# Optimization experiments

Measured on AMD Instinct MI355X. Metric: run time of the kernel, lower is better.

## Reference

```python
import jax, jax.numpy as jnp
import numpy as np

DIM = 192
HEADS = 4
CTX = 256
HID = int(DIM * 2.66)  # 510


def _dwconv(x, w):
    # x: (b,c,h,w), w: (c,1,3,3) depthwise
    return jax.lax.conv_general_dilated(
        x, w, window_strides=(1, 1), padding='SAME',
        dimension_numbers=('NCHW', 'OIHW', 'NCHW'),
        feature_group_count=x.shape[1])


def _conv1x1(x, w):
    # w: (out, in)
    return jnp.einsum('oc,bchw->bohw', w, x)


def _layernorm(x, weight, bias):
    # WithBias LayerNorm over channel dim (last dim after to_3d == channels)
    mu = x.mean(axis=1, keepdims=True)
    var = ((x - mu) ** 2).mean(axis=1, keepdims=True)
    xn = (x - mu) / jnp.sqrt(var + 1e-5)
    return xn * weight[None, :, None, None] + bias[None, :, None, None]


def setup_inputs() -> dict:
    key = jax.random.key(0)
    ks = jax.random.split(key, 16)
    s = 0.02
    inp = {
        'x': jax.random.normal(ks[0], (8, DIM, 128, 128), jnp.float32),
        'context_emb': jax.random.normal(ks[1], (8, CTX), jnp.float32),
        'ln1_w': jnp.ones((DIM,), jnp.float32),
        'ln1_b': jnp.zeros((DIM,), jnp.float32),
        'ln2_w': jnp.ones((DIM,), jnp.float32),
        'ln2_b': jnp.zeros((DIM,), jnp.float32),
        'w_qkv': jax.random.normal(ks[2], (3 * DIM, DIM), jnp.float32) * s,
        'w_qkv_dw': jax.random.normal(ks[3], (3 * DIM, 1, 3, 3), jnp.float32) * s,
        'w_proj': jax.random.normal(ks[4], (DIM, DIM), jnp.float32) * s,
        'base_temp': jnp.ones((HEADS, 1, 1), jnp.float32),
        'ta_w1': jax.random.normal(ks[5], (DIM // 4, CTX), jnp.float32) * s,
        'ta_b1': jnp.zeros((DIM // 4,), jnp.float32),
        'ta_w2': jax.random.normal(ks[6], (HEADS, DIM // 4), jnp.float32) * s,
        'ta_b2': jnp.zeros((HEADS,), jnp.float32),
        'vg_w': jax.random.normal(ks[7], (DIM, CTX), jnp.float32) * s,
        'vg_b': jnp.zeros((DIM,), jnp.float32),
        'w_local': jax.random.normal(ks[8], (DIM, 1, 3, 3), jnp.float32) * s,
        'w_ffn_in': jax.random.normal(ks[9], (2 * HID, DIM), jnp.float32) * s,
        'w_ffn_dw': jax.random.normal(ks[10], (2 * HID, 1, 3, 3), jnp.float32) * s,
        'w_ffn_out': jax.random.normal(ks[11], (DIM, HID), jnp.float32) * s,
    }
    return inp


def _forward(x, context_emb, ln1_w, ln1_b, ln2_w, ln2_b, w_qkv, w_qkv_dw,
             w_proj, base_temp, ta_w1, ta_b1, ta_w2, ta_b2, vg_w, vg_b,
             w_local, w_ffn_in, w_ffn_dw, w_ffn_out):
    b, c, h, w = x.shape
    hd = c // HEADS
    scale = hd ** (-0.5)

    # ---- Attention branch ----
    residual = x
    xn = _layernorm(x, ln1_w, ln1_b)

    # context adapters
    t = jax.nn.relu(context_emb @ ta_w1.T + ta_b1) @ ta_w2.T + ta_b2  # (b,heads)
    temp_factor = jax.nn.sigmoid(t)[:, :, None, None] * 2.0 + 0.5    # (b,heads,1,1)
    total_temp = base_temp[None] * temp_factor
    v_gate = jax.nn.sigmoid(context_emb @ vg_w.T + vg_b)             # (b,dim)
    v_gate = v_gate.reshape(b, HEADS, hd, 1)

    qkv = _dwconv(_conv1x1(xn, w_qkv), w_qkv_dw)
    q, k, v = jnp.split(qkv, 3, axis=1)

    def heads_flat(t4):
        return t4.reshape(b, HEADS, hd, h * w)

    qf = heads_flat(q)
    kf = heads_flat(k)
    vf = heads_flat(v)
    qf = qf / jnp.maximum(jnp.linalg.norm(qf, axis=-1, keepdims=True), 1e-12)
    kf = kf / jnp.maximum(jnp.linalg.norm(kf, axis=-1, keepdims=True), 1e-12)

    attn = jnp.einsum('bhcn,bhdn->bhcd', qf, kf) * scale  # (b,heads,hd,hd)
    attn = jax.nn.softmax(attn * total_temp, axis=-1)

    out_global = jnp.einsum('bhcd,bhdn->bhcn', attn, vf * v_gate)
    out_global = out_global.reshape(b, c, h, w)
    out_local = _dwconv(v, w_local)
    x = residual + _conv1x1(out_global + out_local, w_proj)

    # ---- GDFN branch ----
    residual = x
    xn = _layernorm(x, ln2_w, ln2_b)
    y = _dwconv(_conv1x1(xn, w_ffn_in), w_ffn_dw)
    y1, y2 = jnp.split(y, 2, axis=1)
    y = jax.nn.gelu(y1, approximate=False) * y2
    x = residual + _conv1x1(y, w_ffn_out)
    return x


def reference(x, context_emb, ln1_w, ln1_b, ln2_w, ln2_b, w_qkv, w_qkv_dw,
              w_proj, base_temp, ta_w1, ta_b1, ta_w2, ta_b2, vg_w, vg_b,
              w_local, w_ffn_in, w_ffn_dw, w_ffn_out):
    return _forward(x, context_emb, ln1_w, ln1_b, ln2_w, ln2_b, w_qkv,
                    w_qkv_dw, w_proj, base_temp, ta_w1, ta_b1, ta_w2, ta_b2,
                    vg_w, vg_b, w_local, w_ffn_in, w_ffn_dw, w_ffn_out)
```

## Files before the change

kernel.cpp:

```cpp
#include <hip/hip_runtime.h>
#include <math.h>

#define NB 8
#define NC 192
#define NH 128
#define NW 128
#define HW 16384
#define NQ 576
#define NHID 510
#define NHIDP 512
#define NG2 1020
#define NG2P 1024

#define BROWS 32
#define BSLOTS 34
#define BPIX (BSLOTS * NW)
#define BIPIX (BROWS * NW)

typedef unsigned short u16;
typedef short s16x8 __attribute__((ext_vector_type(8)));
typedef float f32x4 __attribute__((ext_vector_type(4)));

#define MFMA_BF16(a, b, c) __builtin_amdgcn_mfma_f32_16x16x32_bf16((a), (b), (c), 0, 0, 0)

__device__ __forceinline__ u16 f2bf(float f) {
  union { float f; unsigned u; } v; v.f = f;
  unsigned r = v.u + 0x7fffu + ((v.u >> 16) & 1u);
  return (u16)(r >> 16);
}
__device__ __forceinline__ float bf2f(u16 h) {
  union { unsigned u; float f; } v; v.u = ((unsigned)h) << 16; return v.f;
}
__device__ __forceinline__ float lo2f(unsigned u) {
  union { unsigned u; float f; } v; v.u = u << 16; return v.f;
}
__device__ __forceinline__ float hi2f(unsigned u) {
  union { unsigned u; float f; } v; v.u = u & 0xffff0000u; return v.f;
}

__device__ __forceinline__ void gll16(const void* g, void* l) {
  __builtin_amdgcn_global_load_lds(
      (const __attribute__((address_space(1))) void*)g,
      (__attribute__((address_space(3))) void*)l, 16, 0, 0);
}

__global__ void k_prep(const float* __restrict__ wq, const float* __restrict__ wfi,
                       const float* __restrict__ wfo,
                       u16* __restrict__ oq, u16* __restrict__ ofi, u16* __restrict__ ofo) {
  const int n1 = NQ * NC, n2 = NG2P * NC, n3 = NC * NHIDP;
  for (int i = blockIdx.x * blockDim.x + threadIdx.x; i < n1 + n2 + n3;
       i += gridDim.x * blockDim.x) {
    if (i < n1) {
      oq[i] = f2bf(wq[i]);
    } else if (i < n1 + n2) {
      int j = i - n1; int row = j / NC;
      u16 v = 0;
      if (row < NG2) v = f2bf(wfi[j]);
      ofi[j] = v;
    } else {
      int j = i - n1 - n2; int row = j >> 9, col = j & 511;
      u16 v = 0;
      if (col < NHID) v = f2bf(wfo[row * NHID + col]);
      ofo[j] = v;
    }
  }
}

__global__ void k_ctx(const float* __restrict__ ce, const float* __restrict__ taw1,
                      const float* __restrict__ tab1, const float* __restrict__ taw2,
                      const float* __restrict__ tab2, const float* __restrict__ vgw,
                      const float* __restrict__ vgb, const float* __restrict__ btemp,
                      float* __restrict__ tempt, float* __restrict__ vg) {
  int b = blockIdx.x, t = threadIdx.x;
  __shared__ float sce[256];
  __shared__ float shid[48];
  sce[t] = ce[b * 256 + t];
  __syncthreads();
  if (t < 48) {
    float s = tab1[t];
    for (int j = 0; j < 256; j++) s = fmaf(taw1[t * 256 + j], sce[j], s);
    shid[t] = fmaxf(s, 0.f);
  }
  __syncthreads();
  if (t < 4) {
    float s = tab2[t];
    for (int j = 0; j < 48; j++) s = fmaf(taw2[t * 48 + j], shid[j], s);
    float sg = 1.f / (1.f + expf(-s));
    tempt[b * 4 + t] = btemp[t] * (sg * 2.f + 0.5f);
  }
  if (t < 192) {
    float s = vgb[t];
    for (int j = 0; j < 256; j++) s = fmaf(vgw[t * 256 + j], sce[j], s);
    vg[b * 192 + t] = 1.f / (1.f + expf(-s));
  }
}

__global__ __launch_bounds__(256, 2)
void k_ln_gemm_band(const float* __restrict__ in, const float* __restrict__ lnw,
                    const float* __restrict__ lnb, const u16* __restrict__ wbf,
                    u16* __restrict__ out, int nchunks, int row_start, int slot0) {
  __shared__ u16 Xn[64 * 200];
  __shared__ u16 Wc[64 * 200];
  __shared__ float red[512];
  __shared__ float stats[128];
  int t = threadIdx.x;
  int lane = t & 63, wv = t >> 6;
  int bpb = gridDim.x >> 3;
  int b = blockIdx.x / bpb;
  int rb = blockIdx.x - b * bpb;
  int gpx0 = row_start * NW + rb * 64;
  int opx0 = slot0 * NW + rb * 64;
  const float* xp = in + (size_t)b * NC * HW + gpx0 + lane;
  float vals[48];
  float s = 0.f, s2 = 0.f;
#pragma unroll
  for (int j = 0; j < 48; j++) {
    float v = xp[(size_t)(wv * 48 + j) * HW];
    vals[j] = v; s += v; s2 = fmaf(v, v, s2);
  }
  red[wv * 64 + lane] = s;
  red[256 + wv * 64 + lane] = s2;
  __syncthreads();
  if (t < 64) {
    float m = 0.f, q = 0.f;
#pragma unroll
    for (int k = 0; k < 4; k++) { m += red[k * 64 + t]; q += red[256 + k * 64 + t]; }
    m *= (1.f / 192.f);
    float var = q * (1.f / 192.f) - m * m;
    stats[t] = m; stats[64 + t] = rsqrtf(var + 1e-5f);
  }
  __syncthreads();
  float mu = stats[lane], rs = stats[64 + lane];
#pragma unroll
  for (int j = 0; j < 48; j += 2) {
    int c = wv * 48 + j;
    float xa = (vals[j] - mu) * rs * lnw[c] + lnb[c];
    float xb = (vals[j + 1] - mu) * rs * lnw[c + 1] + lnb[c + 1];
    *(unsigned*)&Xn[lane * 200 + c] = (unsigned)f2bf(xa) | ((unsigned)f2bf(xb) << 16);
  }
  int r = lane & 15, grp = lane >> 4;
  int ostride = nchunks << 6;
  for (int nc = 0; nc < nchunks; nc++) {
    __syncthreads();
    for (int i = t; i < 1536; i += 256) {
      int row = i / 24, sg = i % 24;
      *(s16x8*)&Wc[row * 200 + sg * 8] =
          *(const s16x8*)&wbf[(size_t)(nc * 64 + row) * 192 + sg * 8];
    }
    __syncthreads();
    f32x4 z = {0.f, 0.f, 0.f, 0.f};
    f32x4 acc0 = z, acc1 = z, acc2 = z, acc3 = z;
#pragma unroll
    for (int ks = 0; ks < 6; ks++) {
      int k0 = ks * 32 + grp * 8;
      s16x8 a = *(s16x8*)&Xn[(wv * 16 + r) * 200 + k0];
      acc0 = MFMA_BF16(a, *(s16x8*)&Wc[r * 200 + k0], acc0);
      acc1 = MFMA_BF16(a, *(s16x8*)&Wc[(16 + r) * 200 + k0], acc1);
      acc2 = MFMA_BF16(a, *(s16x8*)&Wc[(32 + r) * 200 + k0], acc2);
      acc3 = MFMA_BF16(a, *(s16x8*)&Wc[(48 + r) * 200 + k0], acc3);
    }
    u16* op = out + ((size_t)b * BPIX + opx0 + wv * 16 + grp * 4) * ostride + nc * 64 + r;
#pragma unroll
    for (int i = 0; i < 4; i++) {
      op[(size_t)i * ostride] = f2bf(acc0[i]);
      op[(size_t)i * ostride + 16] = f2bf(acc1[i]);
      op[(size_t)i * ostride + 32] = f2bf(acc2[i]);
      op[(size_t)i * ostride + 48] = f2bf(acc3[i]);
    }
  }
}

__global__ __launch_bounds__(256, 4)
void k_dw_attn_band(const u16* __restrict__ qb_band, const float* __restrict__ wdw,
                    u16* __restrict__ qkb, u16* __restrict__ vpm,
                    float* __restrict__ ssq, int r0, const u16* __restrict__ zp) {
  __shared__ u16 Hl[6 * 18 * 64];
  __shared__ float sred[8 * 64];
  int t = threadIdx.x;
  int cc = blockIdx.x % 9;
  int rem = blockIdx.x / 9;
  int b = rem >> 6; int r2 = rem & 63;
  int h0l = (r2 >> 3) * 4, w0 = (r2 & 7) * 16;
  int c0 = cc * 64;
  const s16x8 z8 = {0, 0, 0, 0, 0, 0, 0, 0};
  for (int i = t; i < 864; i += 256) {
    int px = i >> 3, sg = i & 7;
    int hh = px / 18, ww = px % 18;
    int slot = h0l + hh;
    int gh = r0 - 1 + slot;
    int gw = w0 - 1 + ww;
    const void* g = (gh >= 0 && gh < NH && gw >= 0 && gw < NW)
        ? (const void*)&qb_band[((size_t)b * BPIX + slot * NW + gw) * NQ + c0 + sg * 8]
        : (const void*)zp;
    gll16(g, &Hl[i * 8]);
  }
  __syncthreads();
  int cp = t & 31, psub = t >> 5;
  int pr = psub >> 1, pc0 = (psub & 1) * 8;
  int gc = c0 + 2 * cp;
  float wg0[9], wg1[9];
#pragma unroll
  for (int q = 0; q < 9; q++) { wg0[q] = wdw[gc * 9 + q]; wg1[q] = wdw[(gc + 1) * 9 + q]; }
  bool isv = (c0 >= 384);
  float sq0 = 0.f, sq1 = 0.f;
  s16x8 ov0 = z8, ov1 = z8;
#pragma unroll
  for (int j = 0; j < 8; j++) {
    int pc = pc0 + j;
    float a0 = 0.f, a1 = 0.f;
#pragma unroll
    for (int dr = 0; dr < 3; dr++)
#pragma unroll
      for (int dc = 0; dc < 3; dc++) {
        unsigned u = *(const unsigned*)&Hl[((pr + dr) * 18 + pc + dc) * 64 + 2 * cp];
        a0 = fmaf(lo2f(u), wg0[dr * 3 + dc], a0);
        a1 = fmaf(hi2f(u), wg1[dr * 3 + dc], a1);
      }
    u16 u0 = f2bf(a0), u1 = f2bf(a1);
    if (isv) {
      int gp = (r0 + h0l + pr) * NW + w0 + pc;
      *(unsigned*)&vpm[((size_t)b * HW + gp) * 192 + (gc - 384)] =
          (unsigned)u0 | ((unsigned)u1 << 16);
    } else {
      ov0[j] = (short)u0; ov1[j] = (short)u1;
      float f0 = bf2f(u0), f1 = bf2f(u1);
      sq0 = fmaf(f0, f0, sq0); sq1 = fmaf(f1, f1, sq1);
    }
  }
  if (!isv) {
    int lpx = (h0l + pr) * NW + w0 + pc0;
    *(s16x8*)&qkb[((size_t)b * 384 + gc) * BIPIX + lpx] = ov0;
    *(s16x8*)&qkb[((size_t)b * 384 + gc + 1) * BIPIX + lpx] = ov1;
    sred[psub * 64 + 2 * cp] = sq0;
    sred[psub * 64 + 2 * cp + 1] = sq1;
    __syncthreads();
    if (t < 64) {
      float sa = 0.f;
#pragma unroll
      for (int p8 = 0; p8 < 8; p8++) sa += sred[p8 * 64 + t];
      atomicAdd(&ssq[b * 384 + c0 + t], sa);
    }
  }
}

__global__ __launch_bounds__(256, 2)
void k_attn_band(const u16* __restrict__ qkb, float* __restrict__ attn) {
  __shared__ float par[4 * 2304];
  int t = threadIdx.x;
  int lane = t & 63, wv = t >> 6;
  int r = lane & 15, grp = lane >> 4;
  int bh = blockIdx.x >> 2, kc = blockIdx.x & 3;
  int b = bh >> 2, h = bh & 3;
  const u16* qb = qkb + ((size_t)b * 384 + h * 48) * BIPIX;
  const u16* kb = qkb + ((size_t)b * 384 + 192 + h * 48) * BIPIX;
  f32x4 z = {0.f, 0.f, 0.f, 0.f};
  f32x4 acc[3][3];
#pragma unroll
  for (int i = 0; i < 3; i++)
#pragma unroll
    for (int j = 0; j < 3; j++) acc[i][j] = z;
  int kbase = kc * 1024 + wv * 256 + grp * 8;
#pragma unroll 2
  for (int ks = 0; ks < 8; ks++) {
    int k0 = kbase + ks * 32;
    s16x8 af[3], bf[3];
#pragma unroll
    for (int mt = 0; mt < 3; mt++) af[mt] = *(const s16x8*)&qb[(size_t)(mt * 16 + r) * BIPIX + k0];
#pragma unroll
    for (int nt = 0; nt < 3; nt++) bf[nt] = *(const s16x8*)&kb[(size_t)(nt * 16 + r) * BIPIX + k0];
#pragma unroll
    for (int mt = 0; mt < 3; mt++)
#pragma unroll
      for (int nt = 0; nt < 3; nt++) acc[mt][nt] = MFMA_BF16(af[mt], bf[nt], acc[mt][nt]);
  }
#pragma unroll
  for (int mt = 0; mt < 3; mt++)
#pragma unroll
    for (int nt = 0; nt < 3; nt++)
#pragma unroll
      for (int i = 0; i < 4; i++)
        par[wv * 2304 + (mt * 16 + grp * 4 + i) * 48 + nt * 16 + r] = acc[mt][nt][i];
  __syncthreads();
  float* ag = attn + (size_t)bh * 2304;
  for (int i = t; i < 2304; i += 256)
    atomicAdd(&ag[i], par[i] + par[2304 + i] + par[4608 + i] + par[6912 + i]);
}

__global__ void k_softmax(float* __restrict__ attn, const float* __restrict__ ssq,
                          const float* __restrict__ tempt, const float* __restrict__ vg) {
  int bh = blockIdx.x, b = bh >> 2, h = bh & 3;
  int t = threadIdx.x;
  __shared__ float srk[48], svg[48];
  if (t < 48) {
    float nk = sqrtf(ssq[b * 384 + 192 + h * 48 + t]);
    srk[t] = 1.f / fmaxf(nk, 1e-12f);
    svg[t] = vg[b * 192 + h * 48 + t];
  }
  __syncthreads();
  if (t < 48) {
    float nq = sqrtf(ssq[b * 384 + h * 48 + t]);
    float rq = 1.f / fmaxf(nq, 1e-12f);
    float sc = 0.14433756729740643f * tempt[b * 4 + h] * rq;
    float* row = attn + (size_t)bh * 2304 + t * 48;
    float l[48]; float mx = -1e30f;
#pragma unroll
    for (int d = 0; d < 48; d++) { l[d] = row[d] * srk[d] * sc; mx = fmaxf(mx, l[d]); }
    float ss = 0.f;
#pragma unroll
    for (int d = 0; d < 48; d++) { l[d] = expf(l[d] - mx); ss += l[d]; }
    float inv = 1.f / ss;
#pragma unroll
    for (int d = 0; d < 48; d++) row[d] = l[d] * inv * svg[d];
  }
}

__global__ __launch_bounds__(256)
void k_wd(const float* __restrict__ attn, const float* __restrict__ wp,
          u16* __restrict__ wdg) {
  __shared__ float am[4 * 48 * 48];
  int b = blockIdx.x >> 3, oc = blockIdx.x & 7;
  int t = threadIdx.x;
  const float* ag = attn + (size_t)b * 4 * 2304;
  for (int i = t; i < 9216; i += 256) am[i] = ag[i];
  __syncthreads();
  u16* wdb = wdg + (size_t)b * 192 * 384;
  for (int idx = t; idx < 24 * 384; idx += 256) {
    int oo = idx / 384, j = idx % 384;
    int o = oc * 24 + oo;
    float val;
    if (j < 192) {
      int hj = j / 48, dj = j % 48;
      const float* wpo = wp + o * 192 + hj * 48;
      const float* ap = am + hj * 2304 + dj;
      float sa = 0.f;
#pragma unroll
      for (int c = 0; c < 48; c++) sa = fmaf(wpo[c], ap[c * 48], sa);
      val = sa;
    } else {
      val = wp[o * 192 + (j - 192)];
    }
    wdb[o * 384 + j] = f2bf(val);
  }
}

__global__ __launch_bounds__(256, 2)
void k_proj(const u16* __restrict__ vpm, const float* __restrict__ wl,
            const u16* __restrict__ wdg, const float* __restrict__ x,
            float* __restrict__ x2, const u16* __restrict__ zp) {
  __shared__ u16 Hl[2][6 * 18 * 64];
  __shared__ u16 Xl[64 * 392];
  int t = threadIdx.x;
  int b = blockIdx.x >> 8; int r2 = blockIdx.x & 255;
  int h0 = (r2 >> 3) * 4, w0 = (r2 & 7) * 16;
  int cp = t & 31, psub = t >> 5;
  int pr = psub >> 1, pc0 = (psub & 1) * 8;
  int lane = t & 63, wv = t >> 6;
  int r = lane & 15, grp = lane >> 4;
  float xres[3][4][4];
#pragma unroll
  for (int mt = 0; mt < 3; mt++)
#pragma unroll
    for (int nt = 0; nt < 4; nt++) {
      size_t base = ((size_t)b * NC + wv * 48 + mt * 16 + grp * 4) * HW +
                    (h0 + nt) * NW + w0 + r;
#pragma unroll
      for (int i = 0; i < 4; i++) xres[mt][nt][i] = x[base + (size_t)i * HW];
    }

  auto stageH = [&](int c3s, int buf) {
    int c0s = c3s * 64;
    for (int i = t; i < 864; i += 256) {
      int px = i >> 3, sg = i & 7;
      int hh = px / 18, ww = px % 18;
      int gh = h0 - 1 + hh, gw = w0 - 1 + ww;
      const void* g = (gh >= 0 && gh < NH && gw >= 0 && gw < NW)
          ? (const void*)&vpm[((size_t)b * HW + gh * NW + gw) * 192 + c0s + sg * 8]
          : (const void*)zp;
      gll16(g, &Hl[buf][i * 8]);
    }
  };

  stageH(0, 0);
  __syncthreads();
  int cur = 0;
  for (int c3 = 0; c3 < 3; c3++) {
    if (c3 < 2) stageH(c3 + 1, cur ^ 1);
    int c0 = c3 * 64;
    int gc = c0 + 2 * cp;
    float wg0[9], wg1[9];
#pragma unroll
    for (int q = 0; q < 9; q++) { wg0[q] = wl[gc * 9 + q]; wg1[q] = wl[(gc + 1) * 9 + q]; }
#pragma unroll
    for (int j = 0; j < 8; j++) {
      int pc = pc0 + j; int p = pr * 16 + pc;
      float a0 = 0.f, a1 = 0.f; unsigned uc = 0;
#pragma unroll
      for (int dr = 0; dr < 3; dr++)
#pragma unroll
        for (int dc = 0; dc < 3; dc++) {
          unsigned u = *(const unsigned*)&Hl[cur][((pr + dr) * 18 + pc + dc) * 64 + 2 * cp];
          if (dr == 1 && dc == 1) uc = u;
          a0 = fmaf(lo2f(u), wg0[dr * 3 + dc], a0);
          a1 = fmaf(hi2f(u), wg1[dr * 3 + dc], a1);
        }
      *(unsigned*)&Xl[p * 392 + gc] = uc;
      *(unsigned*)&Xl[p * 392 + 192 + gc] =
          (unsigned)f2bf(a0) | ((unsigned)f2bf(a1) << 16);
    }
    __syncthreads();
    cur ^= 1;
  }
  const u16* wdb = wdg + (size_t)b * 192 * 384;
  f32x4 z = {0.f, 0.f, 0.f, 0.f};
  f32x4 acc[3][4];
#pragma unroll
  for (int i = 0; i < 3; i++)
#pragma unroll
    for (int j = 0; j < 4; j++) acc[i][j] = z;
#pragma unroll 2
  for (int ks = 0; ks < 12; ks++) {
    int k0 = ks * 32 + grp * 8;
    s16x8 b0 = *(s16x8*)&Xl[r * 392 + k0];
    s16x8 b1 = *(s16x8*)&Xl[(16 + r) * 392 + k0];
    s16x8 b2 = *(s16x8*)&Xl[(32 + r) * 392 + k0];
    s16x8 b3 = *(s16x8*)&Xl[(48 + r) * 392 + k0];
#pragma unroll
    for (int mt = 0; mt < 3; mt++) {
      s16x8 a = *(const s16x8*)&wdb[(size_t)(wv * 48 + mt * 16 + r) * 384 + k0];
      acc[mt][0] = MFMA_BF16(a, b0, acc[mt][0]);
      acc[mt][1] = MFMA_BF16(a, b1, acc[mt][1]);
      acc[mt][2] = MFMA_BF16(a, b2, acc[mt][2]);
      acc[mt][3] = MFMA_BF16(a, b3, acc[mt][3]);
    }
  }
#pragma unroll
  for (int mt = 0; mt < 3; mt++)
#pragma unroll
    for (int nt = 0; nt < 4; nt++) {
      size_t base = ((size_t)b * NC + wv * 48 + mt * 16 + grp * 4) * HW +
                    (h0 + nt) * NW + w0 + r;
#pragma unroll
      for (int i = 0; i < 4; i++) {
        size_t idx = base + (size_t)i * HW;
        x2[idx] = acc[mt][nt][i] + xres[mt][nt][i];
      }
    }
}

__global__ __launch_bounds__(256, 2)
void k_gelu_ffn_band(const u16* __restrict__ ypre, const float* __restrict__ wdwf,
                     const u16* __restrict__ wfo, const float* __restrict__ x2,
                     float* __restrict__ out, int r0, const u16* __restrict__ zp) {
  __shared__ u16 H1[2][6 * 18 * 64];
  __shared__ u16 H2[2][6 * 18 * 72];
  __shared__ u16 Yc[64 * 80];
  int t = threadIdx.x;
  int b = blockIdx.x >> 6; int r2 = blockIdx.x & 63;
  int h0l = (r2 >> 3) * 4, w0 = (r2 & 7) * 16;
  int cp = t & 31, psub = t >> 5;
  int pr = psub >> 1, pc0 = (psub & 1) * 8;
  int lane = t & 63, wv = t >> 6;
  int r = lane & 15, grp = lane >> 4;
  int jl = 2 * cp;

  auto stage = [&](int jc, int buf) {
    int j0s = jc * 64;
    int base2 = j0s + 504;
    for (int i = t; i < 864; i += 256) {
      int px = i >> 3, sg = i & 7;
      int hh = px / 18, ww = px % 18;
      int slot = h0l + hh;
      int gh = r0 - 1 + slot, gw = w0 - 1 + ww;
      const void* g = (gh >= 0 && gh < NH && gw >= 0 && gw < NW)
          ? (const void*)&ypre[((size_t)b * BPIX + slot * NW + gw) * NG2P + j0s + sg * 8]
          : (const void*)zp;
      gll16(g, &H1[buf][i * 8]);
    }
    for (int i = t; i < 972; i += 256) {
      int px = i / 9, sg = i - px * 9;
      int hh = px / 18, ww = px % 18;
      int slot = h0l + hh;
      int gh = r0 - 1 + slot, gw = w0 - 1 + ww;
      const void* g = (gh >= 0 && gh < NH && gw >= 0 && gw < NW)
          ? (const void*)&ypre[((size_t)b * BPIX + slot * NW + gw) * NG2P + base2 + sg * 8]
          : (const void*)zp;
      gll16(g, &H2[buf][i * 8]);
    }
  };

  f32x4 z = {0.f, 0.f, 0.f, 0.f};
  f32x4 acc[3][4];
#pragma unroll
  for (int i = 0; i < 3; i++)
#pragma unroll
    for (int j = 0; j < 4; j++) acc[i][j] = z;

  stage(0, 0);
  __syncthreads();
  int cur = 0;
  for (int jc = 0; jc < 8; jc++) {
    if (jc < 7) stage(jc + 1, cur ^ 1);
    int j0 = jc * 64;
    int j = j0 + jl;
    bool v0 = (j < NHID), v1 = (j + 1 < NHID);
    float w1a[9], w1b[9], w2a[9], w2b[9];
#pragma unroll
    for (int q = 0; q < 9; q++) {
      w1a[q] = 0.f; w1b[q] = 0.f; w2a[q] = 0.f; w2b[q] = 0.f;
      if (v0) { w1a[q] = wdwf[j * 9 + q]; w2a[q] = wdwf[(j + NHID) * 9 + q]; }
      if (v1) { w1b[q] = wdwf[(j + 1) * 9 + q]; w2b[q] = wdwf[(j + 1 + NHID) * 9 + q]; }
    }
#pragma unroll
    for (int jj = 0; jj < 8; jj++) {
      int pc = pc0 + jj;
      float d1a = 0.f, d1b = 0.f, d2a = 0.f, d2b = 0.f;
#pragma unroll
      for (int dr = 0; dr < 3; dr++)
#pragma unroll
        for (int dc = 0; dc < 3; dc++) {
          int q = dr * 3 + dc;
          unsigned u1 = *(const unsigned*)&H1[cur][((pr + dr) * 18 + pc + dc) * 64 + jl];
          unsigned u2 = *(const unsigned*)&H2[cur][((pr + dr) * 18 + pc + dc) * 72 + jl + 6];
          d1a = fmaf(lo2f(u1), w1a[q], d1a); d1b = fmaf(hi2f(u1), w1b[q], d1b);
          d2a = fmaf(lo2f(u2), w2a[q], d2a); d2b = fmaf(hi2f(u2), w2b[q], d2b);
        }
      float ga = 0.5f * d1a * (1.f + erff(d1a * 0.70710678118654752f));
      float gb = 0.5f * d1b * (1.f + erff(d1b * 0.70710678118654752f));
      float ya = v0 ? ga * d2a : 0.f;
      float yb = v1 ? gb * d2b : 0.f;
      int lp = pr * 16 + pc;
      *(unsigned*)&Yc[lp * 80 + jl] = (unsigned)f2bf(ya) | ((unsigned)f2bf(yb) << 16);
    }
    __syncthreads();
#pragma unroll
    for (int ks = 0; ks < 2; ks++) {
      int k0 = ks * 32 + grp * 8;
      s16x8 b0 = *(s16x8*)&Yc[r * 80 + k0];
      s16x8 b1 = *(s16x8*)&Yc[(16 + r) * 80 + k0];
      s16x8 b2 = *(s16x8*)&Yc[(32 + r) * 80 + k0];
      s16x8 b3 = *(s16x8*)&Yc[(48 + r) * 80 + k0];
#pragma unroll
      for (int mt = 0; mt < 3; mt++) {
        s16x8 a = *(const s16x8*)&wfo[(size_t)(wv * 48 + mt * 16 + r) * NHIDP + j0 + k0];
        acc[mt][0] = MFMA_BF16(a, b0, acc[mt][0]);
        acc[mt][1] = MFMA_BF16(a, b1, acc[mt][1]);
        acc[mt][2] = MFMA_BF16(a, b2, acc[mt][2]);
        acc[mt][3] = MFMA_BF16(a, b3, acc[mt][3]);
      }
    }
    __syncthreads();
    cur ^= 1;
  }
#pragma unroll
  for (int mt = 0; mt < 3; mt++)
#pragma unroll
    for (int nt = 0; nt < 4; nt++) {
      size_t base = ((size_t)b * NC + wv * 48 + mt * 16 + grp * 4) * HW +
                    (r0 + h0l + nt) * NW + w0 + r;
#pragma unroll
      for (int i = 0; i < 4; i++) {
        size_t idx = base + (size_t)i * HW;
        out[idx] = acc[mt][nt][i] + x2[idx];
      }
    }
}

extern "C" void kernel_launch(void* const* d_in, const int* in_sizes, int n_in,
                              void* d_out, int out_size, void* d_ws, size_t ws_size,
                              hipStream_t stream) {
  const float* x      = (const float*)d_in[0];
  const float* ce     = (const float*)d_in[1];
  const float* ln1w   = (const float*)d_in[2];
  const float* ln1b   = (const float*)d_in[3];
  const float* ln2w   = (const float*)d_in[4];
  const float* ln2b   = (const float*)d_in[5];
  const float* wqkv   = (const float*)d_in[6];
  const float* wqkvdw = (const float*)d_in[7];
  const float* wproj  = (const float*)d_in[8];
  const float* btemp  = (const float*)d_in[9];
  const float* taw1   = (const float*)d_in[10];
  const float* tab1   = (const float*)d_in[11];
  const float* taw2   = (const float*)d_in[12];
  const float* tab2   = (const float*)d_in[13];
  const float* vgw    = (const float*)d_in[14];
  const float* vgb    = (const float*)d_in[15];
  const float* wlocal = (const float*)d_in[16];
  const float* wffni  = (const float*)d_in[17];
  const float* wffndw = (const float*)d_in[18];
  const float* wffno  = (const float*)d_in[19];
  float* outp = (float*)d_out;
  char* ws = (char*)d_ws;

  const size_t REQUIRED = 224602496ULL;
  if (ws_size < REQUIRED) {
    hipMemsetAsync(d_out, 0, (size_t)out_size * 4, stream);
    return;
  }
  u16*   wq_bf   = (u16*)(ws + 0);
  u16*   wfi_bf  = (u16*)(ws + 221184);
  u16*   wfo_bf  = (u16*)(ws + 614400);
  float* tempt   = (float*)(ws + 811008);
  float* vg      = (float*)(ws + 811136);
  float* ssq     = (float*)(ws + 817280);
  float* attn    = (float*)(ws + 829568);
  u16*   wdg     = (u16*)(ws + 1124480);
  u16*   qkvband = (u16*)(ws + 2304128);
  u16*   qkband  = (u16*)(ws + 42412160);
  u16*   ypreband= (u16*)(ws + 2304128);
  u16*   vpm     = (u16*)(ws + 73607296);
  float* x2      = (float*)(ws + 123938944);
  u16*   zp      = (u16*)(ws + 224602240);

  hipMemsetAsync(ws + 817280, 0, 12288 + 294912, stream);
  hipMemsetAsync(ws + 224602240, 0, 256, stream);
  k_prep<<<512, 256, 0, stream>>>(wqkv, wffni, wffno, wq_bf, wfi_bf, wfo_bf);
  k_ctx<<<8, 256, 0, stream>>>(ce, taw1, tab1, taw2, tab2, vgw, vgb, btemp, tempt, vg);

  for (int band = 0; band < 4; band++) {
    int r0 = band * BROWS;
    int rs = (r0 > 0) ? r0 - 1 : 0;
    int re = (r0 + BROWS + 1 < NH) ? r0 + BROWS + 1 : NH;
    int nr = re - rs;
    int s0 = rs - (r0 - 1);
    k_ln_gemm_band<<<8 * nr * 2, 256, 0, stream>>>(x, ln1w, ln1b, wq_bf, qkvband, 9, rs, s0);
    k_dw_attn_band<<<9 * 8 * 64, 256, 0, stream>>>(qkvband, wqkvdw, qkband, vpm, ssq, r0, zp);
    k_attn_band<<<32 * 4, 256, 0, stream>>>(qkband, attn);
  }
  k_softmax<<<32, 64, 0, stream>>>(attn, ssq, tempt, vg);
  k_wd<<<64, 256, 0, stream>>>(attn, wproj, wdg);
  k_proj<<<2048, 256, 0, stream>>>(vpm, wlocal, wdg, x, x2, zp);

  for (int band = 0; band < 4; band++) {
    int r0 = band * BROWS;
    int rs = (r0 > 0) ? r0 - 1 : 0;
    int re = (r0 + BROWS + 1 < NH) ? r0 + BROWS + 1 : NH;
    int nr = re - rs;
    int s0 = rs - (r0 - 1);
    k_ln_gemm_band<<<8 * nr * 2, 256, 0, stream>>>(x2, ln2w, ln2b, wfi_bf, ypreband, 16, rs, s0);
    k_gelu_ffn_band<<<8 * 64, 256, 0, stream>>>(ypreband, wffndw, wfo_bf, x2, outp, r0, zp);
  }
}
```

Baseline: 1.114 ms.

## Double-buffer swizzled weight tiles via async LDS loads; defer residual loads in proj

Weights for the QKV and FFN-in GEMMs are pre-permuted with an XOR swizzle at prep time. This lets k_ln_gemm_band stage each 64-row chunk with global_load_lds into a double-buffered unpadded LDS tile, prefetching the next chunk while computing the current one and avoiding bank conflicts. In k_proj the residual x loads move after the depthwise stage, and an asm barrier pins them in registers, which cuts register pressure during the stencil phase. LDS usage in the GEMM kernel grows, which could reduce occupancy.

```diff
diff --git a/kernel.cpp b/kernel.cpp
--- a/kernel.cpp
+++ b/kernel.cpp
@@ -51,11 +51,16 @@
   for (int i = blockIdx.x * blockDim.x + threadIdx.x; i < n1 + n2 + n3;
        i += gridDim.x * blockDim.x) {
     if (i < n1) {
-      oq[i] = f2bf(wq[i]);
+      int row = i / NC, col = i - row * NC;
+      int g = col >> 3, o = col & 7;
+      int sc = (((g ^ (row & 7)) << 3) | o);
+      oq[i] = f2bf(wq[row * NC + sc]);
     } else if (i < n1 + n2) {
-      int j = i - n1; int row = j / NC;
+      int j = i - n1; int row = j / NC, col = j - row * NC;
+      int g = col >> 3, o = col & 7;
+      int sc = (((g ^ (row & 7)) << 3) | o);
       u16 v = 0;
-      if (row < NG2) v = f2bf(wfi[j]);
+      if (row < NG2) v = f2bf(wfi[row * NC + sc]);
       ofi[j] = v;
     } else {
       int j = i - n1 - n2; int row = j >> 9, col = j & 511;
@@ -100,7 +105,7 @@
                     const float* __restrict__ lnb, const u16* __restrict__ wbf,
                     u16* __restrict__ out, int nchunks, int row_start, int slot0) {
   __shared__ u16 Xn[64 * 200];
-  __shared__ u16 Wc[64 * 200];
+  __shared__ u16 Wc[2][64 * 192];
   __shared__ float red[512];
   __shared__ float stats[128];
   int t = threadIdx.x;
@@ -139,25 +144,31 @@
     *(unsigned*)&Xn[lane * 200 + c] = (unsigned)f2bf(xa) | ((unsigned)f2bf(xb) << 16);
   }
   int r = lane & 15, grp = lane >> 4;
+  int key = r & 7;
   int ostride = nchunks << 6;
+
+  auto stageW = [&](int nc, int buf) {
+    const u16* src = wbf + (size_t)nc * 64 * 192;
+    for (int i = t; i < 1536; i += 256)
+      gll16(&src[i * 8], &Wc[buf][i * 8]);
+  };
+
+  stageW(0, 0);
+  __syncthreads();
+  int cur = 0;
   for (int nc = 0; nc < nchunks; nc++) {
-    __syncthreads();
-    for (int i = t; i < 1536; i += 256) {
-      int row = i / 24, sg = i % 24;
-      *(s16x8*)&Wc[row * 200 + sg * 8] =
-          *(const s16x8*)&wbf[(size_t)(nc * 64 + row) * 192 + sg * 8];
-    }
-    __syncthreads();
+    if (nc + 1 < nchunks) stageW(nc + 1, cur ^ 1);
     f32x4 z = {0.f, 0.f, 0.f, 0.f};
     f32x4 acc0 = z, acc1 = z, acc2 = z, acc3 = z;
 #pragma unroll
     for (int ks = 0; ks < 6; ks++) {
       int k0 = ks * 32 + grp * 8;
+      int gsw = ((((ks << 2) + grp) ^ key) << 3);
       s16x8 a = *(s16x8*)&Xn[(wv * 16 + r) * 200 + k0];
-      acc0 = MFMA_BF16(a, *(s16x8*)&Wc[r * 200 + k0], acc0);
-      acc1 = MFMA_BF16(a, *(s16x8*)&Wc[(16 + r) * 200 + k0], acc1);
-      acc2 = MFMA_BF16(a, *(s16x8*)&Wc[(32 + r) * 200 + k0], acc2);
-      acc3 = MFMA_BF16(a, *(s16x8*)&Wc[(48 + r) * 200 + k0], acc3);
+      acc0 = MFMA_BF16(a, *(s16x8*)&Wc[cur][r * 192 + gsw], acc0);
+      acc1 = MFMA_BF16(a, *(s16x8*)&Wc[cur][(16 + r) * 192 + gsw], acc1);
+      acc2 = MFMA_BF16(a, *(s16x8*)&Wc[cur][(32 + r) * 192 + gsw], acc2);
+      acc3 = MFMA_BF16(a, *(s16x8*)&Wc[cur][(48 + r) * 192 + gsw], acc3);
     }
     u16* op = out + ((size_t)b * BPIX + opx0 + wv * 16 + grp * 4) * ostride + nc * 64 + r;
 #pragma unroll
@@ -167,6 +178,8 @@
       op[(size_t)i * ostride + 32] = f2bf(acc2[i]);
       op[(size_t)i * ostride + 48] = f2bf(acc3[i]);
     }
+    __syncthreads();
+    cur ^= 1;
   }
 }
 
@@ -356,16 +369,6 @@
   int pr = psub >> 1, pc0 = (psub & 1) * 8;
   int lane = t & 63, wv = t >> 6;
   int r = lane & 15, grp = lane >> 4;
-  float xres[3][4][4];
-#pragma unroll
-  for (int mt = 0; mt < 3; mt++)
-#pragma unroll
-    for (int nt = 0; nt < 4; nt++) {
-      size_t base = ((size_t)b * NC + wv * 48 + mt * 16 + grp * 4) * HW +
-                    (h0 + nt) * NW + w0 + r;
-#pragma unroll
-      for (int i = 0; i < 4; i++) xres[mt][nt][i] = x[base + (size_t)i * HW];
-    }
 
   auto stageH = [&](int c3s, int buf) {
     int c0s = c3s * 64;
@@ -410,6 +413,24 @@
     __syncthreads();
     cur ^= 1;
   }
+  float xres[3][4][4];
+#pragma unroll
+  for (int mt = 0; mt < 3; mt++)
+#pragma unroll
+    for (int nt = 0; nt < 4; nt++) {
+      size_t base = ((size_t)b * NC + wv * 48 + mt * 16 + grp * 4) * HW +
+                    (h0 + nt) * NW + w0 + r;
+#pragma unroll
+      for (int i = 0; i < 4; i++) xres[mt][nt][i] = x[base + (size_t)i * HW];
+    }
+#pragma unroll
+  for (int mt = 0; mt < 3; mt++)
+#pragma unroll
+    for (int nt = 0; nt < 4; nt++)
+#pragma unroll
+      for (int i = 0; i < 4; i++)
+        asm volatile("" : "+v"(xres[mt][nt][i]));
+
   const u16* wdb = wdg + (size_t)b * 192 * 384;
   f32x4 z = {0.f, 0.f, 0.f, 0.f};
   f32x4 acc[3][4];
```

Result: faster. 1.077 ms, median of 2 (-3.3%).
